# Performance work log

Measured on AMD Instinct MI355X. Metric: run time of the kernel, lower is better.

The kernel has to match this reference:

```python
import jax, jax.numpy as jnp
import numpy as np


def setup_inputs() -> dict:
    key = jax.random.key(0)
    k1, k2 = jax.random.split(key)
    B, HW, C, M, P = 8, 4096, 1024, 32, 512
    feature_map = jax.random.normal(k1, (B, HW, C), dtype=jnp.float32)
    # normalized (y, x) coords in [0,1], as produced by mask.nonzero()/[H,W]
    point_coords = jax.random.uniform(k2, (B, M, P, 2), dtype=jnp.float32)
    return {"feature_map": feature_map, "point_coords": point_coords}


def reference(feature_map, point_coords):
    # feature_map: [B, H*W, C]; point_coords: [B, M, P, 2] as (y_norm, x_norm).
    B, HW, C = feature_map.shape
    h = w = int(np.sqrt(HW))
    # torch flips coords to (x, y); grid_sample(align_corners=True) maps
    # grid g = 2*coord-1 to pixel coord*(size-1).
    y = point_coords[..., 0] * (h - 1)  # [B, M, P]
    x = point_coords[..., 1] * (w - 1)
    x0f = jnp.floor(x)
    y0f = jnp.floor(y)
    wx = (x - x0f)[..., None]  # [B, M, P, 1]
    wy = (y - y0f)[..., None]
    ix0 = jnp.clip(x0f.astype(jnp.int32), 0, w - 1)
    ix1 = jnp.clip(ix0 + 1, 0, w - 1)
    iy0 = jnp.clip(y0f.astype(jnp.int32), 0, h - 1)
    iy1 = jnp.clip(iy0 + 1, 0, h - 1)

    def gather(iy, ix):
        idx = (iy * w + ix).reshape(B, -1)  # [B, M*P]
        g = jnp.take_along_axis(feature_map, idx[:, :, None], axis=1)  # [B, M*P, C]
        return g.reshape(B, iy.shape[1], iy.shape[2], C)

    f00 = gather(iy0, ix0)
    f01 = gather(iy0, ix1)
    f10 = gather(iy1, ix0)
    f11 = gather(iy1, ix1)
    # bilinear interpolation -> [B, M, P, C]
    sampled = (f00 * (1 - wx) * (1 - wy) + f01 * wx * (1 - wy)
               + f10 * (1 - wx) * wy + f11 * wx * wy)
    # AdaptiveAvgPool1d(1) over points, then transpose -> [B, M, 1, C]
    region_feat = jnp.mean(sampled, axis=2, keepdims=True)
    return region_feat
```

## Files before the change

### kernel.cpp

```cpp
#include <hip/hip_runtime.h>


#define NB 8
#define NM 32
#define NP 512
#define NC 1024
#define NH 64
#define NHW 4096

#define KC   64
#define NKC  (NHW / KC)
#define CT   256
#define NCT  (NC / CT)

__global__ __launch_bounds__(256) void scatter_w(
    const float* __restrict__ pc, float* __restrict__ W)
{
    int idx = blockIdx.x * 256 + threadIdx.x;
    int bm  = idx >> 9;
    int m   = bm & (NM - 1);
    int b   = bm >> 5;

    float2 c = ((const float2*)pc)[idx];
    float y = c.x * 63.0f;
    float x = c.y * 63.0f;
    float x0f = floorf(x), y0f = floorf(y);
    float wx = x - x0f, wy = y - y0f;
    int ix0 = min(max((int)x0f, 0), 63);
    int ix1 = min(ix0 + 1, 63);
    int iy0 = min(max((int)y0f, 0), 63);
    int iy1 = min(iy0 + 1, 63);
    float wx1 = 1.0f - wx, wy1 = 1.0f - wy;
    const float s = 1.0f / (float)NP;

    float* Wb = W + (size_t)b * (NHW * NM) + m;
    atomicAdd(Wb + ((iy0 * NH + ix0) * NM), wx1 * wy1 * s);
    atomicAdd(Wb + ((iy0 * NH + ix1) * NM), wx  * wy1 * s);
    atomicAdd(Wb + ((iy1 * NH + ix0) * NM), wx1 * wy  * s);
    atomicAdd(Wb + ((iy1 * NH + ix1) * NM), wx  * wy  * s);
}

__global__ __launch_bounds__(256, 8) void wgemm(
    const float* __restrict__ W, const float* __restrict__ F,
    float* __restrict__ out)
{
    __shared__ float4 sW[KC * NM / 4];

    const int kc  = blockIdx.x;
    const int ct  = blockIdx.y;
    const int b   = blockIdx.z;
    const int tid = threadIdx.x;
    const int c   = ct * CT + tid;
    const int hw0 = kc * KC;

    const float4* Wg = (const float4*)(W + ((size_t)b * NHW + hw0) * NM);
    sW[tid]       = Wg[tid];
    sW[tid + 256] = Wg[tid + 256];
    __syncthreads();

    const float* Fb = F + ((size_t)b * NHW + hw0) * NC + c;

    float acc[NM];
#pragma unroll
    for (int m = 0; m < NM; ++m) acc[m] = 0.0f;

#pragma unroll 4
    for (int i = 0; i < KC; ++i) {
        float f = Fb[(size_t)i * NC];
        const float4* w4 = sW + i * (NM / 4);
#pragma unroll
        for (int mq = 0; mq < NM / 4; ++mq) {
            float4 w = w4[mq];
            acc[mq * 4 + 0] = fmaf(w.x, f, acc[mq * 4 + 0]);
            acc[mq * 4 + 1] = fmaf(w.y, f, acc[mq * 4 + 1]);
            acc[mq * 4 + 2] = fmaf(w.z, f, acc[mq * 4 + 2]);
            acc[mq * 4 + 3] = fmaf(w.w, f, acc[mq * 4 + 3]);
        }
    }

    float* ob = out + (size_t)b * (NM * NC) + c;
#pragma unroll
    for (int m = 0; m < NM; ++m)
        atomicAdd(ob + (size_t)m * NC, acc[m]);
}

__global__ __launch_bounds__(256) void region_pool_direct(
    const float* __restrict__ fm, const float* __restrict__ pc,
    float* __restrict__ out)
{
    __shared__ int4   sIdx[NP];
    __shared__ float4 sWt[NP];
    const int bid = blockIdx.x;
    const int b   = bid >> 5;
    const int tid = threadIdx.x;
    const float2* pc2 = (const float2*)(pc + (size_t)bid * NP * 2);
    for (int p = tid; p < NP; p += 256) {
        float2 c = pc2[p];
        float y = c.x * 63.0f, x = c.y * 63.0f;
        float x0f = floorf(x), y0f = floorf(y);
        float wx = x - x0f, wy = y - y0f;
        int ix0 = min(max((int)x0f, 0), 63);
        int ix1 = min(ix0 + 1, 63);
        int iy0 = min(max((int)y0f, 0), 63);
        int iy1 = min(iy0 + 1, 63);
        sIdx[p] = make_int4((iy0 * NH + ix0) << 10, (iy0 * NH + ix1) << 10,
                            (iy1 * NH + ix0) << 10, (iy1 * NH + ix1) << 10);
        float wx1 = 1.0f - wx, wy1 = 1.0f - wy;
        sWt[p] = make_float4(wx1 * wy1, wx * wy1, wx1 * wy, wx * wy);
    }
    __syncthreads();
    const float* Fb = fm + (size_t)b * (NHW * NC) + tid * 4;
    float4 acc = make_float4(0.f, 0.f, 0.f, 0.f);
#pragma unroll 4
    for (int p = 0; p < NP; ++p) {
        int4 off = sIdx[p]; float4 w = sWt[p];
        float4 f00 = *(const float4*)(Fb + off.x);
        float4 f01 = *(const float4*)(Fb + off.y);
        float4 f10 = *(const float4*)(Fb + off.z);
        float4 f11 = *(const float4*)(Fb + off.w);
        acc.x = fmaf(w.x, f00.x, fmaf(w.y, f01.x, fmaf(w.z, f10.x, fmaf(w.w, f11.x, acc.x))));
        acc.y = fmaf(w.x, f00.y, fmaf(w.y, f01.y, fmaf(w.z, f10.y, fmaf(w.w, f11.y, acc.y))));
        acc.z = fmaf(w.x, f00.z, fmaf(w.y, f01.z, fmaf(w.z, f10.z, fmaf(w.w, f11.z, acc.z))));
        acc.w = fmaf(w.x, f00.w, fmaf(w.y, f01.w, fmaf(w.z, f10.w, fmaf(w.w, f11.w, acc.w))));
    }
    const float inv = 1.0f / (float)NP;
    ((float4*)(out + (size_t)bid * NC))[tid] =
        make_float4(acc.x * inv, acc.y * inv, acc.z * inv, acc.w * inv);
}

extern "C" void kernel_launch(void* const* d_in, const int* in_sizes, int n_in,
                              void* d_out, int out_size, void* d_ws, size_t ws_size,
                              hipStream_t stream) {
    const float* fm = (const float*)d_in[0];
    const float* pc = (const float*)d_in[1];
    float* out = (float*)d_out;

    const size_t wbytes = (size_t)NB * NHW * NM * sizeof(float);
    if (ws_size >= wbytes) {
        float* W = (float*)d_ws;
        hipMemsetAsync(W, 0, wbytes, stream);
        hipMemsetAsync(out, 0, (size_t)out_size * sizeof(float), stream);
        scatter_w<<<(NB * NM * NP) / 256, 256, 0, stream>>>(pc, W);
        dim3 grid(NKC, NCT, NB);
        wgemm<<<grid, CT, 0, stream>>>(W, fm, out);
    } else {
        region_pool_direct<<<NB * NM, 256, 0, stream>>>(fm, pc, out);
    }
}
```

Before: 274.5 us.

## Enlarge K chunk, prefetch feature rows, replace output atomics with partial-sum reduction

The weighted-GEMM kernel now processes 256 spatial positions per block instead of 64, cutting the grid to 16 K-chunks. Feature loads are software-prefetched in groups of 8 to hide global latency. The per-element atomicAdd into the output is replaced by writing per-chunk partial sums to workspace, followed by a separate reduction kernel. This removes atomic contention and the output memset, but adds a second kernel, extra workspace traffic, and lower occupancy from larger shared memory and higher register use.

```diff
diff --git a/kernel.cpp b/kernel.cpp
--- a/kernel.cpp
+++ b/kernel.cpp
@@ -8,10 +8,11 @@
 #define NH 64
 #define NHW 4096
 
-#define KC   64
+#define KC   256
 #define NKC  (NHW / KC)
 #define CT   256
 #define NCT  (NC / CT)
+#define PF   8
 
 __global__ __launch_bounds__(256) void scatter_w(
     const float* __restrict__ pc, float* __restrict__ W)
@@ -40,9 +41,9 @@
     atomicAdd(Wb + ((iy1 * NH + ix1) * NM), wx  * wy  * s);
 }
 
-__global__ __launch_bounds__(256, 8) void wgemm(
+__global__ __launch_bounds__(256, 2) void wgemm(
     const float* __restrict__ W, const float* __restrict__ F,
-    float* __restrict__ out)
+    float* __restrict__ P)
 {
     __shared__ float4 sW[KC * NM / 4];
 
@@ -54,8 +55,9 @@
     const int hw0 = kc * KC;
 
     const float4* Wg = (const float4*)(W + ((size_t)b * NHW + hw0) * NM);
-    sW[tid]       = Wg[tid];
-    sW[tid + 256] = Wg[tid + 256];
+#pragma unroll
+    for (int j = 0; j < 8; ++j)
+        sW[tid + 256 * j] = Wg[tid + 256 * j];
     __syncthreads();
 
     const float* Fb = F + ((size_t)b * NHW + hw0) * NC + c;
@@ -64,24 +66,53 @@
 #pragma unroll
     for (int m = 0; m < NM; ++m) acc[m] = 0.0f;
 
-#pragma unroll 4
-    for (int i = 0; i < KC; ++i) {
-        float f = Fb[(size_t)i * NC];
-        const float4* w4 = sW + i * (NM / 4);
+    float fbuf[PF];
 #pragma unroll
-        for (int mq = 0; mq < NM / 4; ++mq) {
-            float4 w = w4[mq];
-            acc[mq * 4 + 0] = fmaf(w.x, f, acc[mq * 4 + 0]);
-            acc[mq * 4 + 1] = fmaf(w.y, f, acc[mq * 4 + 1]);
-            acc[mq * 4 + 2] = fmaf(w.z, f, acc[mq * 4 + 2]);
-            acc[mq * 4 + 3] = fmaf(w.w, f, acc[mq * 4 + 3]);
+    for (int j = 0; j < PF; ++j) fbuf[j] = Fb[(size_t)j * NC];
+
+    for (int i = 0; i < KC; i += PF) {
+        float fcur[PF];
+#pragma unroll
+        for (int j = 0; j < PF; ++j) fcur[j] = fbuf[j];
+        if (i + PF < KC) {
+#pragma unroll
+            for (int j = 0; j < PF; ++j)
+                fbuf[j] = Fb[(size_t)(i + PF + j) * NC];
+        }
+#pragma unroll
+        for (int j = 0; j < PF; ++j) {
+            const float4* w4 = sW + (i + j) * (NM / 4);
+            float f = fcur[j];
+#pragma unroll
+            for (int mq = 0; mq < NM / 4; ++mq) {
+                float4 w = w4[mq];
+                acc[mq * 4 + 0] = fmaf(w.x, f, acc[mq * 4 + 0]);
+                acc[mq * 4 + 1] = fmaf(w.y, f, acc[mq * 4 + 1]);
+                acc[mq * 4 + 2] = fmaf(w.z, f, acc[mq * 4 + 2]);
+                acc[mq * 4 + 3] = fmaf(w.w, f, acc[mq * 4 + 3]);
+            }
         }
     }
 
-    float* ob = out + (size_t)b * (NM * NC) + c;
+    float* pb = P + (((size_t)kc * NB + b) * NM) * NC + c;
 #pragma unroll
     for (int m = 0; m < NM; ++m)
-        atomicAdd(ob + (size_t)m * NC, acc[m]);
+        pb[(size_t)m * NC] = acc[m];
+}
+
+__global__ __launch_bounds__(256) void reduce_p(
+    const float* __restrict__ P, float* __restrict__ out)
+{
+    const int idx = blockIdx.x * 256 + threadIdx.x;
+    const float4* p4 = (const float4*)P;
+    const int stride = NB * NM * NC / 4;
+    float4 s = make_float4(0.f, 0.f, 0.f, 0.f);
+#pragma unroll
+    for (int kc = 0; kc < NKC; ++kc) {
+        float4 v = p4[(size_t)kc * stride + idx];
+        s.x += v.x; s.y += v.y; s.z += v.z; s.w += v.w;
+    }
+    ((float4*)out)[idx] = s;
 }
 
 __global__ __launch_bounds__(256) void region_pool_direct(
@@ -136,13 +167,15 @@
     float* out = (float*)d_out;
 
     const size_t wbytes = (size_t)NB * NHW * NM * sizeof(float);
-    if (ws_size >= wbytes) {
+    const size_t pbytes = (size_t)NKC * NB * NM * NC * sizeof(float);
+    if (ws_size >= wbytes + pbytes) {
         float* W = (float*)d_ws;
+        float* P = (float*)((char*)d_ws + wbytes);
         hipMemsetAsync(W, 0, wbytes, stream);
-        hipMemsetAsync(out, 0, (size_t)out_size * sizeof(float), stream);
         scatter_w<<<(NB * NM * NP) / 256, 256, 0, stream>>>(pc, W);
         dim3 grid(NKC, NCT, NB);
-        wgemm<<<grid, CT, 0, stream>>>(W, fm, out);
+        wgemm<<<grid, CT, 0, stream>>>(W, fm, P);
+        reduce_p<<<(NB * NM * NC / 4) / 256, 256, 0, stream>>>(P, out);
     } else {
         region_pool_direct<<<NB * NM, 256, 0, stream>>>(fm, pc, out);
     }
```

New measurement: 233.1 us. 15.1% less time.
